# Optimization experiments

Measured on AMD Instinct MI355X. Metric: run time of the kernel, lower is better.

Reference implementation:

```python
import jax, jax.numpy as jnp
from jax import lax
import numpy as np

# module hyper-parameters (init_kwargs)
TOPK, NEIGHBOR, NEGATIVE, THRESH = 5, 16, 16, 0.5


def setup_inputs() -> dict:
    key = jax.random.key(0)
    k1, k2, k3, k4 = jax.random.split(key, 4)
    B, N, D = 32, 64, 512
    score_pred = jax.random.normal(k1, (B, N, N), jnp.float32)
    # valid proposals: end column >= start row (upper-triangular 2D temporal map)
    map2d_mask = jnp.triu(jnp.ones((N, N), dtype=bool))
    map2d = jax.random.normal(k2, (B, N, N, D), jnp.float32)
    offset_gt = jax.random.normal(k3, (B, N, N, 2), jnp.float32)
    tmap = jax.random.uniform(k4, (B, N, N), jnp.float32)
    return dict(score_pred=score_pred, map2d_mask=map2d_mask, map2d=map2d,
                offset_gt=offset_gt, tmap=tmap)


def _iou_1d(m, ref):
    # m: [M,2] int (start,end), ref: [2] int -> temporal IoU, float32
    inter = jnp.clip(jnp.minimum(m[:, 1], ref[1]) - jnp.maximum(m[:, 0], ref[0]), 0)
    union = jnp.maximum(m[:, 1], ref[1]) - jnp.minimum(m[:, 0], ref[0])
    return inter.astype(jnp.float32) / union.astype(jnp.float32)


def _select_one(scores, moments):
    """proposal_selection_with_negative for one batch element.
    scores: [M] float, moments: [M,2] int. Returns K=NEGATIVE+TOPK*(NEIGHBOR+1)
    indices into the ORIGINAL (unsorted) proposal list."""
    M = moments.shape[0]
    total = TOPK * (NEIGHBOR + 1)
    order = jnp.argsort(-scores)            # descending score order
    m = moments[order]                      # [M,2] sorted moments
    ar = jnp.arange(M)

    # sequential NMS-style suppression; stops after TOPK picks (or i==M-1)
    def cond(st):
        i, cnt, _, _ = st
        return (cnt < TOPK) & (i < M - 1)

    def body(st):
        i, cnt, sup, sel = st
        mask = (_iou_1d(m, m[i]) > THRESH) & (ar > i)          # neighbors of head i
        nb = mask & (jnp.cumsum(mask) <= NEIGHBOR)             # first NEIGHBOR of them
        free = ~sup[i]
        sup = jnp.where(free, sup | mask | (ar == i), sup)
        sel = jnp.where(free, sel | nb | (ar == i), sel)
        return (i + 1, cnt + free.astype(jnp.int32), sup, sel)

    _, _, sup, sel = lax.while_loop(
        cond, body,
        (jnp.int32(0), jnp.int32(0), jnp.zeros(M, bool), jnp.zeros(M, bool)))

    n_sel = sel.sum()
    unsup = ~sup
    n_unsup = unsup.sum()
    sel_idx = jnp.nonzero(sel, size=total, fill_value=M - 1)[0]     # sorted-order positions
    unsup_idx = jnp.nonzero(unsup, size=M, fill_value=M - 1)[0]

    # negatives = flip(moments[~suppressed])[:NEGATIVE] -> last NEGATIVE unsuppressed, reversed
    j = jnp.arange(NEGATIVE)
    neg_idx = unsup_idx[jnp.clip(n_unsup - 1 - j, 0, M - 1)]
    # if fewer than `total` selected, pad with head of unsuppressed (placed BEFORE selected)
    pad = total - n_sel
    p = jnp.arange(total)
    mid_idx = jnp.where(p < pad, unsup_idx[p],
                        sel_idx[jnp.clip(p - pad, 0, total - 1)])
    idx_sorted = jnp.concatenate([neg_idx, mid_idx])                # [K] sorted-order positions
    return order[idx_sorted]                                        # back to original order


def reference(score_pred, map2d_mask, map2d, offset_gt, tmap):
    B, N = score_pred.shape[0], score_pred.shape[1]
    M = N * (N + 1) // 2  # static count of valid cells (upper-triangular mask)
    rows, cols = jnp.nonzero(map2d_mask, size=M, fill_value=0)
    moments = jnp.stack([rows, cols + 1], axis=1)   # [M,2] (start, end)
    scores = score_pred[:, rows, cols]              # [B,M]

    idx = jax.vmap(lambda s: _select_one(s, moments))(scores)  # [B,K]
    r, c = rows[idx], cols[idx]                     # [B,K] grid coords
    K = idx.shape[1]
    bix = jnp.arange(B)[:, None]

    prop_feature = map2d[bix, r, c].reshape(B * K, -1)          # [B*K, D]
    pred_s_e = jnp.stack([r, c + 1], axis=-1).reshape(B * K, 2) # [B*K, 2] int
    offset_sel = offset_gt[bix, r, c].reshape(B * K, 2)         # [B*K, 2]
    pred_score = tmap[bix, r, c].reshape(B * K)                 # [B*K]
    return prop_feature, pred_s_e, offset_sel, pred_score
```

## Files before the change

kernel.cpp:

```cpp
#include <hip/hip_runtime.h>
#include <math.h>
#include <stdint.h>

#define N_      64
#define M_      2080
#define SORTN   4096
#define B_      32
#define TOPK_   5
#define NEIGH_  16
#define NEG_    16
#define TOTAL_  85
#define KOUT_   101
#define D_      512
#define NT_     1024
#define NWAVE_  (NT_ / 64)
#define CHUNK_  3

__device__ __forceinline__ int block_scan_excl(int v, int tid, int* s_wsum)
{
    __syncthreads();
    const int lane = tid & 63;
    const int wave = tid >> 6;
    int x = v;
#pragma unroll
    for (int off = 1; off < 64; off <<= 1) {
        int y = __shfl_up(x, off);
        if (lane >= off) x += y;
    }
    if (lane == 63) s_wsum[wave] = x;
    __syncthreads();
    if (wave == 0) {
        int w = (lane < NWAVE_) ? s_wsum[lane] : 0;
#pragma unroll
        for (int off = 1; off < NWAVE_; off <<= 1) {
            int y = __shfl_up(w, off);
            if (lane >= off) w += y;
        }
        if (lane < NWAVE_) s_wsum[lane] = w;
    }
    __syncthreads();
    int base = (wave > 0) ? s_wsum[wave - 1] : 0;
    return base + x - v;
}

__global__ __launch_bounds__(NT_) void select_kernel(
    const float* __restrict__ score_pred,
    const float* __restrict__ offset_gt,
    const float* __restrict__ tmap,
    float* __restrict__ out_pse,
    float* __restrict__ out_off,
    float* __restrict__ out_score)
{
    __shared__ uint64_t s_kv[SORTN];
    __shared__ unsigned char s_r[M_], s_c[M_];
    __shared__ unsigned char sm_s[M_], sm_e[M_];
    __shared__ unsigned char s_sup[M_], s_sel[M_];
    __shared__ int s_unsupidx[M_];
    __shared__ int s_selidx[TOTAL_];
    __shared__ int s_wsum[NWAVE_];

    const int b   = blockIdx.x;
    const int tid = threadIdx.x;

    if (tid < N_) {
        int r  = tid;
        int rs = r * N_ - (r * (r - 1)) / 2;
        for (int k = 0; k < N_ - r; ++k) {
            s_r[rs + k] = (unsigned char)r;
            s_c[rs + k] = (unsigned char)(r + k);
        }
    }
    __syncthreads();

    const float* sp = score_pred + (size_t)b * N_ * N_;
    for (int m = tid; m < SORTN; m += NT_) {
        uint64_t kv;
        if (m < M_) {
            int r = s_r[m], c = s_c[m];
            uint32_t fb  = __float_as_uint(sp[r * N_ + c]);
            uint32_t ord = (fb & 0x80000000u) ? ~fb : (fb | 0x80000000u);
            uint32_t dk  = ~ord;
            kv = ((uint64_t)dk << 32) | (uint32_t)m;
        } else {
            kv = ~0ULL;
        }
        s_kv[m] = kv;
    }
    __syncthreads();

    for (int kk = 2; kk <= SORTN; kk <<= 1) {
        for (int j = kk >> 1; j > 0; j >>= 1) {
            const int jm = j - 1;
            int p0 = tid;
            int p1 = tid + NT_;
            int i0 = ((p0 & ~jm) << 1) | (p0 & jm);
            int i1 = ((p1 & ~jm) << 1) | (p1 & jm);
            uint64_t a0 = s_kv[i0], b0 = s_kv[i0 + j];
            uint64_t a1 = s_kv[i1], b1 = s_kv[i1 + j];
            bool up0 = ((i0 & kk) == 0);
            bool up1 = ((i1 & kk) == 0);
            bool sw0 = up0 ? (a0 > b0) : (a0 < b0);
            bool sw1 = up1 ? (a1 > b1) : (a1 < b1);
            if (sw0) { s_kv[i0] = b0; s_kv[i0 + j] = a0; }
            if (sw1) { s_kv[i1] = b1; s_kv[i1 + j] = a1; }
            __syncthreads();
        }
    }

    for (int jj = tid; jj < M_; jj += NT_) {
        int o = (int)(uint32_t)s_kv[jj];
        sm_s[jj] = s_r[o];
        sm_e[jj] = (unsigned char)(s_c[o] + 1);
        s_sup[jj] = 0;
        s_sel[jj] = 0;
        s_unsupidx[jj] = M_ - 1;
    }
    if (tid < TOTAL_) s_selidx[tid] = M_ - 1;
    __syncthreads();

    const int j0 = tid * CHUNK_;
    int i = 0, cnt = 0;
    while (cnt < TOPK_ && i < M_ - 1) {
        bool freei = (s_sup[i] == 0);
        if (freei) {
            const int si = sm_s[i], ei = sm_e[i];
            unsigned int mkbits = 0;
            int localcnt = 0;
#pragma unroll
            for (int t = 0; t < CHUNK_; ++t) {
                int jj = j0 + t;
                if (jj < M_ && jj > i) {
                    int s = sm_s[jj], e = sm_e[jj];
                    int inter = (e < ei ? e : ei) - (s > si ? s : si);
                    int uni   = (e > ei ? e : ei) - (s < si ? s : si);
                    if (inter > 0 && 2 * inter > uni) {
                        mkbits |= (1u << t);
                        ++localcnt;
                    }
                }
            }
            int run = block_scan_excl(localcnt, tid, s_wsum);
#pragma unroll
            for (int t = 0; t < CHUNK_; ++t) {
                if (mkbits & (1u << t)) {
                    int jj = j0 + t;
                    s_sup[jj] = 1;
                    if (run < NEIGH_) s_sel[jj] = 1;
                    ++run;
                }
            }
            if (tid == 0) { s_sup[i] = 1; s_sel[i] = 1; }
            ++cnt;
        }
        ++i;
        __syncthreads();
    }

    int n_sel, n_unsup;
    {
        int localcnt = 0;
#pragma unroll
        for (int t = 0; t < CHUNK_; ++t) {
            int jj = j0 + t;
            if (jj < M_) localcnt += s_sel[jj];
        }
        int run = block_scan_excl(localcnt, tid, s_wsum);
        n_sel = s_wsum[NWAVE_ - 1];
#pragma unroll
        for (int t = 0; t < CHUNK_; ++t) {
            int jj = j0 + t;
            if (jj < M_ && s_sel[jj]) {
                if (run < TOTAL_) s_selidx[run] = jj;
                ++run;
            }
        }
    }
    {
        int localcnt = 0;
#pragma unroll
        for (int t = 0; t < CHUNK_; ++t) {
            int jj = j0 + t;
            if (jj < M_) localcnt += (s_sup[jj] == 0);
        }
        int run = block_scan_excl(localcnt, tid, s_wsum);
        n_unsup = s_wsum[NWAVE_ - 1];
#pragma unroll
        for (int t = 0; t < CHUNK_; ++t) {
            int jj = j0 + t;
            if (jj < M_ && s_sup[jj] == 0) {
                s_unsupidx[run] = jj;
                ++run;
            }
        }
    }
    __syncthreads();

    if (tid < KOUT_) {
        int idx_sorted;
        if (tid < NEG_) {
            int t = n_unsup - 1 - tid;
            if (t < 0) t = 0;
            idx_sorted = s_unsupidx[t];
        } else {
            int p   = tid - NEG_;
            int pad = TOTAL_ - n_sel;
            idx_sorted = (p < pad) ? s_unsupidx[p] : s_selidx[p - pad];
        }
        int o = (int)(uint32_t)s_kv[idx_sorted];
        int r = s_r[o], c = s_c[o];
        int gk = b * KOUT_ + tid;
        out_pse[2 * gk + 0] = (float)r;
        out_pse[2 * gk + 1] = (float)(c + 1);
        const float* og = offset_gt + ((size_t)b * N_ * N_ + r * N_ + c) * 2;
        out_off[2 * gk + 0] = og[0];
        out_off[2 * gk + 1] = og[1];
        out_score[gk] = tmap[(size_t)b * N_ * N_ + r * N_ + c];
    }
}

__global__ __launch_bounds__(128) void gather_kernel(
    const float* __restrict__ map2d,
    const float* __restrict__ out_pse,
    float* __restrict__ out_feat)
{
    int gk = blockIdx.x;
    int b  = gk / KOUT_;
    int r  = (int)out_pse[2 * gk + 0];
    int c  = (int)out_pse[2 * gk + 1] - 1;
    const float4* src = (const float4*)(map2d + ((size_t)b * N_ * N_ + r * N_ + c) * D_);
    float4*       dst = (float4*)(out_feat + (size_t)gk * D_);
    dst[threadIdx.x] = src[threadIdx.x];
}

extern "C" void kernel_launch(void* const* d_in, const int* in_sizes, int n_in,
                              void* d_out, int out_size, void* d_ws, size_t ws_size,
                              hipStream_t stream)
{
    const float* score_pred = (const float*)d_in[0];
    const float* map2d      = (const float*)d_in[2];
    const float* offset_gt  = (const float*)d_in[3];
    const float* tmap       = (const float*)d_in[4];

    float* out       = (float*)d_out;
    float* out_feat  = out;
    float* out_pse   = out_feat + (size_t)B_ * KOUT_ * D_;
    float* out_off   = out_pse  + (size_t)B_ * KOUT_ * 2;
    float* out_score = out_off  + (size_t)B_ * KOUT_ * 2;

    select_kernel<<<B_, NT_, 0, stream>>>(score_pred, offset_gt, tmap,
                                          out_pse, out_off, out_score);
    gather_kernel<<<B_ * KOUT_, 128, 0, stream>>>(map2d, out_pse, out_feat);
}
```

Before: 346.8 us.

## Move bitonic sort into registers with wave shuffles for small strides

Each thread keeps four sort keys in registers instead of shared memory. Compare-exchange stages with stride under 64 use wave-level xor shuffles, and the two largest strides are done inside each thread's registers. Only the mid-range strides go through shared memory, each with two barriers. The aim is to cut the many per-stage __syncthreads and shared-memory round trips in the block-wide sort, at the cost of more register pressure and 64-bit shuffles split into two 32-bit ones.

New measurement: 349.7 us. No clear change (+0.8%).

```diff
diff --git a/kernel.cpp b/kernel.cpp
--- a/kernel.cpp
+++ b/kernel.cpp
@@ -15,6 +15,21 @@
 #define NT_     1024
 #define NWAVE_  (NT_ / 64)
 #define CHUNK_  3
+#define VPT_    4
+
+__device__ __forceinline__ uint64_t shfl_xor_u64(uint64_t x, int mask)
+{
+    int lo = __shfl_xor((int)(uint32_t)x, mask);
+    int hi = __shfl_xor((int)(uint32_t)(x >> 32), mask);
+    return ((uint64_t)(uint32_t)hi << 32) | (uint32_t)lo;
+}
+
+__device__ __forceinline__ void cas2(uint64_t& a, uint64_t& b, bool up)
+{
+    bool sw = up ? (a > b) : (a < b);
+    uint64_t t = a;
+    if (sw) { a = b; b = t; }
+}
 
 __device__ __forceinline__ int block_scan_excl(int v, int tid, int* s_wsum)
 {
@@ -73,40 +88,61 @@
     __syncthreads();
 
     const float* sp = score_pred + (size_t)b * N_ * N_;
-    for (int m = tid; m < SORTN; m += NT_) {
-        uint64_t kv;
-        if (m < M_) {
-            int r = s_r[m], c = s_c[m];
+    uint64_t v[VPT_];
+#pragma unroll
+    for (int k = 0; k < VPT_; ++k) {
+        int g = k * NT_ + tid;
+        if (g < M_) {
+            int r = s_r[g], c = s_c[g];
             uint32_t fb  = __float_as_uint(sp[r * N_ + c]);
             uint32_t ord = (fb & 0x80000000u) ? ~fb : (fb | 0x80000000u);
             uint32_t dk  = ~ord;
-            kv = ((uint64_t)dk << 32) | (uint32_t)m;
+            v[k] = ((uint64_t)dk << 32) | (uint32_t)g;
         } else {
-            kv = ~0ULL;
-        }
-        s_kv[m] = kv;
-    }
-    __syncthreads();
+            v[k] = ~0ULL;
+        }
+    }
 
     for (int kk = 2; kk <= SORTN; kk <<= 1) {
         for (int j = kk >> 1; j > 0; j >>= 1) {
-            const int jm = j - 1;
-            int p0 = tid;
-            int p1 = tid + NT_;
-            int i0 = ((p0 & ~jm) << 1) | (p0 & jm);
-            int i1 = ((p1 & ~jm) << 1) | (p1 & jm);
-            uint64_t a0 = s_kv[i0], b0 = s_kv[i0 + j];
-            uint64_t a1 = s_kv[i1], b1 = s_kv[i1 + j];
-            bool up0 = ((i0 & kk) == 0);
-            bool up1 = ((i1 & kk) == 0);
-            bool sw0 = up0 ? (a0 > b0) : (a0 < b0);
-            bool sw1 = up1 ? (a1 > b1) : (a1 < b1);
-            if (sw0) { s_kv[i0] = b0; s_kv[i0 + j] = a0; }
-            if (sw1) { s_kv[i1] = b1; s_kv[i1 + j] = a1; }
-            __syncthreads();
-        }
-    }
-
+            if (j == 2048) {
+                cas2(v[0], v[2], true);
+                cas2(v[1], v[3], true);
+            } else if (j == 1024) {
+                cas2(v[0], v[1], true);
+                cas2(v[2], v[3], kk == SORTN);
+            } else if (j >= 64) {
+                __syncthreads();
+#pragma unroll
+                for (int k = 0; k < VPT_; ++k)
+                    s_kv[k * NT_ + tid] = v[k];
+                __syncthreads();
+#pragma unroll
+                for (int k = 0; k < VPT_; ++k) {
+                    int g = k * NT_ + tid;
+                    uint64_t o = s_kv[g ^ j];
+                    bool up    = ((g & kk) == 0);
+                    bool keepS = (((g & j) == 0) == up);
+                    v[k] = ((v[k] < o) == keepS) ? v[k] : o;
+                }
+            } else {
+#pragma unroll
+                for (int k = 0; k < VPT_; ++k) {
+                    int g = k * NT_ + tid;
+                    uint64_t o = shfl_xor_u64(v[k], j);
+                    bool up    = ((g & kk) == 0);
+                    bool keepS = (((tid & j) == 0) == up);
+                    v[k] = ((v[k] < o) == keepS) ? v[k] : o;
+                }
+            }
+        }
+    }
+
+    __syncthreads();
+#pragma unroll
+    for (int k = 0; k < VPT_; ++k)
+        s_kv[k * NT_ + tid] = v[k];
+    __syncthreads();
     for (int jj = tid; jj < M_; jj += NT_) {
         int o = (int)(uint32_t)s_kv[jj];
         sm_s[jj] = s_r[o];
```

## Replace bitonic sort with LDS radix sort and single-wave NMS loop

Applied to the files above, without the earlier changes.

Swaps the 4096-element shared-memory bitonic sort, which needs many block-wide barriers, for a 4-pass 8-bit LSD radix sort on the upper 32 key bits. Each pass ranks elements with wave ballots and does a per-digit prefix scan. Because the low bits are the unique original index, this still gives a stable descending order. The NMS suppression loop now runs on a single wavefront using ballots and popcount instead of block scans with barriers per iteration, and it jumps straight to the next unsuppressed head. In exchange it uses more LDS and one wave walks all proposals serially.

Measured after the change: 354.6 us. 1.02x slower.

```diff
diff --git a/kernel.cpp b/kernel.cpp
--- a/kernel.cpp
+++ b/kernel.cpp
@@ -4,7 +4,6 @@
 
 #define N_      64
 #define M_      2080
-#define SORTN   4096
 #define B_      32
 #define TOPK_   5
 #define NEIGH_  16
@@ -13,8 +12,10 @@
 #define KOUT_   101
 #define D_      512
 #define NT_     1024
-#define NWAVE_  (NT_ / 64)
+#define NWAVE_  16
 #define CHUNK_  3
+#define NE_     3072
+#define KPT_    3
 
 __device__ __forceinline__ int block_scan_excl(int v, int tid, int* s_wsum)
 {
@@ -51,7 +52,10 @@
     float* __restrict__ out_off,
     float* __restrict__ out_score)
 {
-    __shared__ uint64_t s_kv[SORTN];
+    __shared__ uint64_t s_a[NE_];
+    __shared__ uint64_t s_b[NE_];
+    __shared__ __align__(16) int s_cnt[256 * 48];
+    __shared__ int s_dbase[256];
     __shared__ unsigned char s_r[M_], s_c[M_];
     __shared__ unsigned char sm_s[M_], sm_e[M_];
     __shared__ unsigned char s_sup[M_], s_sel[M_];
@@ -59,8 +63,11 @@
     __shared__ int s_selidx[TOTAL_];
     __shared__ int s_wsum[NWAVE_];
 
-    const int b   = blockIdx.x;
-    const int tid = threadIdx.x;
+    const int b    = blockIdx.x;
+    const int tid  = threadIdx.x;
+    const int lane = tid & 63;
+    const int wav  = tid >> 6;
+    const uint64_t ltmask = (1ULL << lane) - 1ULL;
 
     if (tid < N_) {
         int r  = tid;
@@ -73,42 +80,102 @@
     __syncthreads();
 
     const float* sp = score_pred + (size_t)b * N_ * N_;
-    for (int m = tid; m < SORTN; m += NT_) {
+#pragma unroll
+    for (int k = 0; k < KPT_; ++k) {
+        int g = k * NT_ + tid;
         uint64_t kv;
-        if (m < M_) {
-            int r = s_r[m], c = s_c[m];
-            uint32_t fb  = __float_as_uint(sp[r * N_ + c]);
+        if (g < M_) {
+            uint32_t fb  = __float_as_uint(sp[s_r[g] * N_ + s_c[g]]);
             uint32_t ord = (fb & 0x80000000u) ? ~fb : (fb | 0x80000000u);
             uint32_t dk  = ~ord;
-            kv = ((uint64_t)dk << 32) | (uint32_t)m;
+            kv = ((uint64_t)dk << 32) | (uint32_t)g;
         } else {
             kv = ~0ULL;
         }
-        s_kv[m] = kv;
-    }
-    __syncthreads();
-
-    for (int kk = 2; kk <= SORTN; kk <<= 1) {
-        for (int j = kk >> 1; j > 0; j >>= 1) {
-            const int jm = j - 1;
-            int p0 = tid;
-            int p1 = tid + NT_;
-            int i0 = ((p0 & ~jm) << 1) | (p0 & jm);
-            int i1 = ((p1 & ~jm) << 1) | (p1 & jm);
-            uint64_t a0 = s_kv[i0], b0 = s_kv[i0 + j];
-            uint64_t a1 = s_kv[i1], b1 = s_kv[i1 + j];
-            bool up0 = ((i0 & kk) == 0);
-            bool up1 = ((i1 & kk) == 0);
-            bool sw0 = up0 ? (a0 > b0) : (a0 < b0);
-            bool sw1 = up1 ? (a1 > b1) : (a1 < b1);
-            if (sw0) { s_kv[i0] = b0; s_kv[i0 + j] = a0; }
-            if (sw1) { s_kv[i1] = b1; s_kv[i1 + j] = a1; }
-            __syncthreads();
-        }
-    }
+        s_a[g] = kv;
+    }
+
+    uint64_t* cur = s_a;
+    uint64_t* dst = s_b;
+#pragma unroll
+    for (int pass = 0; pass < 4; ++pass) {
+        const int shift = 32 + 8 * pass;
+        __syncthreads();
+
+        {
+            int4* z = (int4*)s_cnt;
+#pragma unroll
+            for (int q = 0; q < 3; ++q)
+                z[q * NT_ + tid] = make_int4(0, 0, 0, 0);
+        }
+
+        uint64_t kv[KPT_];
+        int dg[KPT_], rk[KPT_];
+#pragma unroll
+        for (int k = 0; k < KPT_; ++k) {
+            kv[k] = cur[k * NT_ + tid];
+            dg[k] = (int)((kv[k] >> shift) & 0xFF);
+        }
+        __syncthreads();
+
+#pragma unroll
+        for (int k = 0; k < KPT_; ++k) {
+            int d = dg[k];
+            uint64_t m = ~0ULL;
+#pragma unroll
+            for (int bit = 0; bit < 8; ++bit) {
+                uint64_t bal = __ballot((d >> bit) & 1);
+                m &= ((d >> bit) & 1) ? bal : ~bal;
+            }
+            rk[k] = __popcll(m & ltmask);
+            if (rk[k] == 0)
+                s_cnt[d * 48 + k * 16 + wav] = __popcll(m);
+        }
+        __syncthreads();
+
+        int dig_tot = 0, dig_incl = 0;
+        if (tid < 256) {
+            int vals[48];
+#pragma unroll
+            for (int q = 0; q < 48; ++q) vals[q] = s_cnt[tid * 48 + q];
+            int run = 0;
+#pragma unroll
+            for (int q = 0; q < 48; ++q) {
+                int c = vals[q];
+                s_cnt[tid * 48 + q] = run;
+                run += c;
+            }
+            dig_tot  = run;
+            dig_incl = run;
+#pragma unroll
+            for (int off = 1; off < 64; off <<= 1) {
+                int y = __shfl_up(dig_incl, off);
+                if (lane >= off) dig_incl += y;
+            }
+            if (lane == 63) s_wsum[wav] = dig_incl;
+        }
+        __syncthreads();
+        if (tid < 256) {
+            int base = 0;
+#pragma unroll
+            for (int q = 0; q < 4; ++q)
+                if (q < wav) base += s_wsum[q];
+            s_dbase[tid] = base + dig_incl - dig_tot;
+        }
+        __syncthreads();
+
+#pragma unroll
+        for (int k = 0; k < KPT_; ++k) {
+            int d   = dg[k];
+            int off = s_dbase[d] + s_cnt[d * 48 + k * 16 + wav] + rk[k];
+            dst[off] = kv[k];
+        }
+        uint64_t* t = cur; cur = dst; dst = t;
+    }
+    __syncthreads();
 
     for (int jj = tid; jj < M_; jj += NT_) {
-        int o = (int)(uint32_t)s_kv[jj];
+        int o = (int)(uint32_t)cur[jj];
         sm_s[jj] = s_r[o];
         sm_e[jj] = (unsigned char)(s_c[o] + 1);
         s_sup[jj] = 0;
@@ -118,44 +185,50 @@
     if (tid < TOTAL_) s_selidx[tid] = M_ - 1;
     __syncthreads();
 
-    const int j0 = tid * CHUNK_;
-    int i = 0, cnt = 0;
-    while (cnt < TOPK_ && i < M_ - 1) {
-        bool freei = (s_sup[i] == 0);
-        if (freei) {
+    if (tid < 64) {
+        volatile unsigned char* vsup = s_sup;
+        volatile unsigned char* vsel = s_sel;
+        int i = 0, cnt = 0;
+        for (;;) {
             const int si = sm_s[i], ei = sm_e[i];
-            unsigned int mkbits = 0;
-            int localcnt = 0;
-#pragma unroll
-            for (int t = 0; t < CHUNK_; ++t) {
-                int jj = j0 + t;
+            int run = 0;
+#pragma unroll 1
+            for (int q = 0; q < (M_ + 63) / 64; ++q) {
+                int jj = q * 64 + lane;
+                bool match = false;
                 if (jj < M_ && jj > i) {
                     int s = sm_s[jj], e = sm_e[jj];
                     int inter = (e < ei ? e : ei) - (s > si ? s : si);
                     int uni   = (e > ei ? e : ei) - (s < si ? s : si);
-                    if (inter > 0 && 2 * inter > uni) {
-                        mkbits |= (1u << t);
-                        ++localcnt;
-                    }
+                    match = (inter > 0 && 2 * inter > uni);
                 }
-            }
-            int run = block_scan_excl(localcnt, tid, s_wsum);
-#pragma unroll
-            for (int t = 0; t < CHUNK_; ++t) {
-                if (mkbits & (1u << t)) {
-                    int jj = j0 + t;
-                    s_sup[jj] = 1;
-                    if (run < NEIGH_) s_sel[jj] = 1;
-                    ++run;
+                uint64_t bal = __ballot(match);
+                if (match) {
+                    int pre = run + __popcll(bal & ltmask);
+                    vsup[jj] = 1;
+                    if (pre < NEIGH_) vsel[jj] = 1;
                 }
-            }
-            if (tid == 0) { s_sup[i] = 1; s_sel[i] = 1; }
+                run += __popcll(bal);
+            }
+            if (lane == 0) { vsup[i] = 1; vsel[i] = 1; }
             ++cnt;
-        }
-        ++i;
-        __syncthreads();
-    }
-
+            if (cnt >= TOPK_) break;
+            int next = -1;
+            int base = i + 1;
+            while (base < M_ - 1) {
+                int jj = base + lane;
+                bool freep = (jj < M_ - 1) && (vsup[jj] == 0);
+                uint64_t bal = __ballot(freep);
+                if (bal) { next = base + (__ffsll((long long)bal) - 1); break; }
+                base += 64;
+            }
+            if (next < 0) break;
+            i = next;
+        }
+    }
+    __syncthreads();
+
+    const int j0 = tid * CHUNK_;
     int n_sel, n_unsup;
     {
         int localcnt = 0;
@@ -206,7 +279,7 @@
             int pad = TOTAL_ - n_sel;
             idx_sorted = (p < pad) ? s_unsupidx[p] : s_selidx[p - pad];
         }
-        int o = (int)(uint32_t)s_kv[idx_sorted];
+        int o = (int)(uint32_t)cur[idx_sorted];
         int r = s_r[o], c = s_c[o];
         int gk = b * KOUT_ + tid;
         out_pse[2 * gk + 0] = (float)r;
```
